# Optimization experiments

Measured on AMD Instinct MI355X. Metric: run time of the kernel, lower is better.

Reference implementation:

```python
import jax, jax.numpy as jnp
import numpy as np

N = 50000      # nodes
E = 500000     # edges
IN = 128       # input feature dim
HID = 64       # hidden per-head dim
CLS = 64       # num classes
SLOPE = 0.2    # leaky_relu negative slope


def _gat_layer(x, W, al, ar, src, dst):
    """One GATConv: project, per-edge score, edge-softmax over dst, weighted aggregate.
    x: [N, Din], W: [Din, H*F], al/ar: [H, F]. Returns [N, H, F]."""
    H, F = al.shape
    n = x.shape[0]
    feat = (x @ W).reshape(n, H, F)                      # [N,H,F]
    el = jnp.einsum('nhf,hf->nh', feat, al)              # [N,H]
    er = jnp.einsum('nhf,hf->nh', feat, ar)              # [N,H]
    e = el[src] + er[dst]                                # u_add_v -> [E,H]
    e = jnp.where(e >= 0, e, SLOPE * e)                  # leaky_relu
    # edge_softmax over destination nodes (numerically stable)
    m = jax.lax.stop_gradient(jax.ops.segment_max(e, dst, num_segments=n))
    ex = jnp.exp(e - m[dst])
    denom = jax.ops.segment_sum(ex, dst, num_segments=n)
    a = ex / denom[dst]                                  # [E,H]
    # u_mul_e + sum aggregation
    out = jax.ops.segment_sum(feat[src] * a[:, :, None], dst, num_segments=n)
    return out                                           # [N,H,F]


def setup_inputs() -> dict:
    key = jax.random.key(0)
    ks = jax.random.split(key, 12)
    s = 0.05  # xavier-ish scale
    x = jax.random.normal(ks[0], (N, IN), jnp.float32)
    src = jax.random.randint(ks[1], (E,), 0, N)
    dst = jax.random.randint(ks[2], (E,), 0, N)
    W1 = jax.random.normal(ks[3], (IN, 4 * HID), jnp.float32) * s
    al1 = jax.random.normal(ks[4], (4, HID), jnp.float32) * s
    ar1 = jax.random.normal(ks[5], (4, HID), jnp.float32) * s
    W2 = jax.random.normal(ks[6], (4 * HID, 4 * HID), jnp.float32) * s
    al2 = jax.random.normal(ks[7], (4, HID), jnp.float32) * s
    ar2 = jax.random.normal(ks[8], (4, HID), jnp.float32) * s
    W3 = jax.random.normal(ks[9], (4 * HID, CLS), jnp.float32) * s
    al3 = jax.random.normal(ks[10], (1, CLS), jnp.float32) * s
    ar3 = jax.random.normal(ks[11], (1, CLS), jnp.float32) * s
    res_W3 = jax.random.normal(jax.random.fold_in(key, 99), (4 * HID, CLS), jnp.float32) * s
    return {"x": x, "W1": W1, "al1": al1, "ar1": ar1, "W2": W2, "al2": al2,
            "ar2": ar2, "W3": W3, "al3": al3, "ar3": ar3, "res_W3": res_W3,
            "src": src, "dst": dst}


def reference(x, W1, al1, ar1, W2, al2, ar2, W3, al3, ar3, res_W3, src, dst):
    # layer 0: no residual, elu activation, flatten heads
    h = _gat_layer(x, W1, al1, ar1, src, dst)            # [N,4,64]
    h = jax.nn.elu(h).reshape(N, -1)                     # [N,256]
    # layer 1: residual is Identity (in_dst 256 == 4*64), elu, flatten
    h1 = _gat_layer(h, W2, al2, ar2, src, dst)           # [N,4,64]
    h1 = h1 + h.reshape(N, 4, HID)                       # residual (Identity)
    h = jax.nn.elu(h1).reshape(N, -1)                    # [N,256]
    # layer 2: residual Linear 256->64, no activation, mean over heads
    h2 = _gat_layer(h, W3, al3, ar3, src, dst)           # [N,1,64]
    h2 = h2 + (h @ res_W3).reshape(N, 1, CLS)            # residual fc
    logits = h2.mean(axis=1)                             # [N,64]
    return logits
```

## Files before the change

### kernel.cpp

```cpp
#include <hip/hip_runtime.h>
#include <hip/hip_bf16.h>
#include <math.h>

#define SLOPE 0.2f

typedef __attribute__((ext_vector_type(8))) short short8;
typedef __attribute__((ext_vector_type(4))) float f32x4;

static __device__ __forceinline__ float leakyf(float x) { return x >= 0.f ? x : SLOPE * x; }
static __device__ __forceinline__ float bflo(unsigned u) { return __builtin_bit_cast(float, u << 16); }
static __device__ __forceinline__ float bfhi(unsigned u) { return __builtin_bit_cast(float, u & 0xffff0000u); }
static __device__ __forceinline__ unsigned short f2bf(float f) {
    unsigned u = __builtin_bit_cast(unsigned, f);
    return (unsigned short)((u + 0x7fff + ((u >> 16) & 1)) >> 16);
}

struct __align__(8) us4 { unsigned short a, b, c, d; };

__global__ __launch_bounds__(256) void tconv_all(const float* __restrict__ W1,
                                                 const float* __restrict__ W2,
                                                 const float* __restrict__ W3,
                                                 const float* __restrict__ rW3,
                                                 unsigned short* __restrict__ W1t,
                                                 unsigned short* __restrict__ W2t,
                                                 unsigned short* __restrict__ W3c) {
    int i = blockIdx.x * 256 + threadIdx.x;
    const float* W; unsigned short* Wt; int K, lNc, idx;
    if (i < 32768)       { W = W1;  Wt = W1t;            K = 128; lNc = 8; idx = i; }
    else if (i < 98304)  { W = W2;  Wt = W2t;            K = 256; lNc = 8; idx = i - 32768; }
    else if (i < 114688) { W = W3;  Wt = W3c;            K = 256; lNc = 6; idx = i - 98304; }
    else                 { W = rW3; Wt = W3c + 64 * 256; K = 256; lNc = 6; idx = i - 114688; }
    int k = idx >> lNc, n = idx & ((1 << lNc) - 1);
    Wt[n * K + k] = f2bf(W[idx]);
}

template<bool A_F32>
__global__ __launch_bounds__(256) void gemm_l12(const void* __restrict__ Av,
                                                const unsigned short* __restrict__ Wt,
                                                unsigned short* __restrict__ outb,
                                                const float* __restrict__ al,
                                                const float* __restrict__ ar,
                                                float* __restrict__ el,
                                                float* __restrict__ er,
                                                int M, int K) {
    const int lane = threadIdx.x & 63;
    const int wid = threadIdx.x >> 6;
    const int rlo = lane & 15;
    const int q = lane >> 4;
    const int kg = q * 8;
    const int m0 = blockIdx.x * 64;
    const int cbase = wid * 64;

    f32x4 acc[4][4];
#pragma unroll
    for (int mf = 0; mf < 4; ++mf)
#pragma unroll
        for (int nf = 0; nf < 4; ++nf) acc[mf][nf] = (f32x4){0.f, 0.f, 0.f, 0.f};

    for (int k0 = 0; k0 < K; k0 += 32) {
        short8 a[4];
#pragma unroll
        for (int mf = 0; mf < 4; ++mf) {
            int r = m0 + mf * 16 + rlo;
            if (r >= M) r = M - 1;
            if (A_F32) {
                const float* ap = (const float*)Av + (size_t)r * K + k0 + kg;
                float4 f0 = *(const float4*)ap;
                float4 f1 = *(const float4*)(ap + 4);
                short8 t;
                t[0] = f2bf(f0.x); t[1] = f2bf(f0.y); t[2] = f2bf(f0.z); t[3] = f2bf(f0.w);
                t[4] = f2bf(f1.x); t[5] = f2bf(f1.y); t[6] = f2bf(f1.z); t[7] = f2bf(f1.w);
                a[mf] = t;
            } else {
                a[mf] = *(const short8*)((const unsigned short*)Av + (size_t)r * K + k0 + kg);
            }
        }
#pragma unroll
        for (int nf = 0; nf < 4; ++nf) {
            short8 b = *(const short8*)(Wt + (size_t)(cbase + nf * 16 + rlo) * K + k0 + kg);
#pragma unroll
            for (int mf = 0; mf < 4; ++mf)
                acc[mf][nf] = __builtin_amdgcn_mfma_f32_16x16x32_bf16(a[mf], b, acc[mf][nf], 0, 0, 0);
        }
    }

    float alv[4], arv[4];
#pragma unroll
    for (int nf = 0; nf < 4; ++nf) {
        alv[nf] = al[cbase + nf * 16 + rlo];
        arv[nf] = ar[cbase + nf * 16 + rlo];
    }

#pragma unroll
    for (int mf = 0; mf < 4; ++mf) {
#pragma unroll
        for (int reg = 0; reg < 4; ++reg) {
            int r = m0 + mf * 16 + q * 4 + reg;
            float pl = 0.f, pr = 0.f;
#pragma unroll
            for (int nf = 0; nf < 4; ++nf) {
                pl += acc[mf][nf][reg] * alv[nf];
                pr += acc[mf][nf][reg] * arv[nf];
            }
#pragma unroll
            for (int off = 1; off < 16; off <<= 1) {
                pl += __shfl_xor(pl, off);
                pr += __shfl_xor(pr, off);
            }
            if (rlo == 0 && r < M) {
                el[(size_t)r * 4 + wid] = pl;
                er[(size_t)r * 4 + wid] = pr;
            }
            if (r < M) {
#pragma unroll
                for (int nf = 0; nf < 4; ++nf)
                    outb[(size_t)r * 256 + cbase + nf * 16 + rlo] = f2bf(acc[mf][nf][reg]);
            }
        }
    }
}

__global__ __launch_bounds__(256) void gemm_l3(const unsigned short* __restrict__ A,
                                               const unsigned short* __restrict__ Wt,
                                               unsigned short* __restrict__ featb,
                                               float* __restrict__ resf,
                                               const float* __restrict__ al,
                                               const float* __restrict__ ar,
                                               float* __restrict__ el,
                                               float* __restrict__ er, int M) {
    const int K = 256;
    const int lane = threadIdx.x & 63;
    const int wid = threadIdx.x >> 6;
    const int rlo = lane & 15;
    const int q = lane >> 4;
    const int kg = q * 8;
    const int m0 = blockIdx.x * 128 + (wid >> 1) * 64;
    const int ch = wid & 1;
    const int cbase = ch * 64;

    f32x4 acc[4][4];
#pragma unroll
    for (int mf = 0; mf < 4; ++mf)
#pragma unroll
        for (int nf = 0; nf < 4; ++nf) acc[mf][nf] = (f32x4){0.f, 0.f, 0.f, 0.f};

    for (int k0 = 0; k0 < K; k0 += 32) {
        short8 a[4];
#pragma unroll
        for (int mf = 0; mf < 4; ++mf) {
            int r = m0 + mf * 16 + rlo;
            if (r >= M) r = M - 1;
            a[mf] = *(const short8*)(A + (size_t)r * K + k0 + kg);
        }
#pragma unroll
        for (int nf = 0; nf < 4; ++nf) {
            short8 b = *(const short8*)(Wt + (size_t)(cbase + nf * 16 + rlo) * K + k0 + kg);
#pragma unroll
            for (int mf = 0; mf < 4; ++mf)
                acc[mf][nf] = __builtin_amdgcn_mfma_f32_16x16x32_bf16(a[mf], b, acc[mf][nf], 0, 0, 0);
        }
    }

    float alv[4], arv[4];
    if (ch == 0) {
#pragma unroll
        for (int nf = 0; nf < 4; ++nf) {
            alv[nf] = al[nf * 16 + rlo];
            arv[nf] = ar[nf * 16 + rlo];
        }
    }

#pragma unroll
    for (int mf = 0; mf < 4; ++mf) {
#pragma unroll
        for (int reg = 0; reg < 4; ++reg) {
            int r = m0 + mf * 16 + q * 4 + reg;
            if (ch == 0) {
                float pl = 0.f, pr = 0.f;
#pragma unroll
                for (int nf = 0; nf < 4; ++nf) {
                    pl += acc[mf][nf][reg] * alv[nf];
                    pr += acc[mf][nf][reg] * arv[nf];
                }
#pragma unroll
                for (int off = 1; off < 16; off <<= 1) {
                    pl += __shfl_xor(pl, off);
                    pr += __shfl_xor(pr, off);
                }
                if (rlo == 0 && r < M) { el[r] = pl; er[r] = pr; }
                if (r < M) {
#pragma unroll
                    for (int nf = 0; nf < 4; ++nf)
                        featb[(size_t)r * 64 + nf * 16 + rlo] = f2bf(acc[mf][nf][reg]);
                }
            } else if (r < M) {
#pragma unroll
                for (int nf = 0; nf < 4; ++nf)
                    resf[(size_t)r * 64 + nf * 16 + rlo] = acc[mf][nf][reg];
            }
        }
    }
}

__global__ void hist_kernel(const int* __restrict__ dst, int* __restrict__ counts, int e) {
    int i = blockIdx.x * blockDim.x + threadIdx.x;
    if (i < e) atomicAdd(&counts[dst[i]], 1);
}

__global__ __launch_bounds__(1024) void scan_block(const int* __restrict__ counts,
                                                   int* __restrict__ offsets,
                                                   int* __restrict__ bsums, int n) {
    __shared__ int ws[16];
    int tid = threadIdx.x, lane = tid & 63, wid = tid >> 6;
    int idx = blockIdx.x * 1024 + tid;
    int v = (idx < n) ? counts[idx] : 0;
    int s = v;
#pragma unroll
    for (int off = 1; off < 64; off <<= 1) {
        int t = __shfl_up(s, off);
        if (lane >= off) s += t;
    }
    if (lane == 63) ws[wid] = s;
    __syncthreads();
    if (tid < 16) {
        int w2 = ws[tid];
#pragma unroll
        for (int off = 1; off < 16; off <<= 1) {
            int t = __shfl_up(w2, off);
            if (tid >= off) w2 += t;
        }
        ws[tid] = w2;
    }
    __syncthreads();
    int wpre = wid ? ws[wid - 1] : 0;
    if (idx < n) offsets[idx] = wpre + s - v;
    if (tid == 0) bsums[blockIdx.x] = ws[15];
}

__global__ __launch_bounds__(1024) void add_off(const int* __restrict__ bsums,
                                                int* __restrict__ offsets,
                                                int* __restrict__ cursor, int n, int e, int nb) {
    __shared__ int base_s;
    int tid = threadIdx.x;
    if (tid < 64) {
        int v = (tid < blockIdx.x && tid < nb) ? bsums[tid] : 0;
#pragma unroll
        for (int off = 32; off > 0; off >>= 1) v += __shfl_xor(v, off);
        if (tid == 0) base_s = v;
    }
    __syncthreads();
    int idx = blockIdx.x * 1024 + tid;
    if (idx < n) {
        int v = offsets[idx] + base_s;
        offsets[idx] = v;
        cursor[idx] = v;
    }
    if (idx == 0) offsets[n] = e;
}

__global__ void scatter_kernel(const int* __restrict__ src, const int* __restrict__ dst,
                               int* __restrict__ cursor, int* __restrict__ csr_src,
                               int* __restrict__ csr_dst, int e) {
    int i = blockIdx.x * blockDim.x + threadIdx.x;
    if (i < e) {
        int d = dst[i];
        int pos = atomicAdd(&cursor[d], 1);
        csr_src[pos] = src[i];
        csr_dst[pos] = d;
    }
}

template<int H>
__global__ __launch_bounds__(256) void edge_scores(const int* __restrict__ csr_src,
                                                   const int* __restrict__ csr_dst,
                                                   const float* __restrict__ el,
                                                   const float* __restrict__ er,
                                                   float* __restrict__ w, int E) {
    int e = blockIdx.x * 256 + threadIdx.x;
    if (e >= E) return;
    int s = csr_src[e], d = csr_dst[e];
    if (H == 4) {
        float4 l = *(const float4*)(el + (size_t)s * 4);
        float4 r = *(const float4*)(er + (size_t)d * 4);
        float4 o;
        o.x = __expf(fminf(leakyf(l.x + r.x), 80.f));
        o.y = __expf(fminf(leakyf(l.y + r.y), 80.f));
        o.z = __expf(fminf(leakyf(l.z + r.z), 80.f));
        o.w = __expf(fminf(leakyf(l.w + r.w), 80.f));
        *(float4*)(w + (size_t)e * 4) = o;
    } else {
        w[e] = __expf(fminf(leakyf(el[s] + er[d]), 80.f));
    }
}

template<int H, int RES, int ACT, bool OUT_BF16>
__global__ __launch_bounds__(256) void gat_agg(const unsigned short* __restrict__ fp,
                                               const float* __restrict__ wbuf,
                                               const int* __restrict__ offsets,
                                               const int* __restrict__ csr_src,
                                               const void* __restrict__ resid,
                                               void* __restrict__ outv, int n) {
    const int D = H * 64;
    int node = blockIdx.x * 4 + (threadIdx.x >> 6);
    int lane = threadIdx.x & 63;
    if (node >= n) return;
    int e0 = offsets[node], e1 = offsets[node + 1];
    const int hf = (H == 4) ? (lane >> 4) : 0;

    float den = 0.f;
    float acc[4] = {0.f, 0.f, 0.f, 0.f};

    for (int e = e0; e < e1; e += 8) {
        int s[8];
        float w[8];
#pragma unroll
        for (int j = 0; j < 8; ++j) {
            int idx = e + j;
            bool ok = idx < e1;
            int ii = ok ? idx : (e1 - 1);
            s[j] = csr_src[ii];
            float wv = (H == 4) ? wbuf[(size_t)ii * 4 + hf] : wbuf[ii];
            w[j] = ok ? wv : 0.f;
        }
        if (H == 4) {
            uint2 u[8];
#pragma unroll
            for (int j = 0; j < 8; ++j)
                u[j] = *(const uint2*)(fp + (size_t)s[j] * 256 + lane * 4);
#pragma unroll
            for (int j = 0; j < 8; ++j) {
                den += w[j];
                acc[0] += w[j] * bflo(u[j].x);
                acc[1] += w[j] * bfhi(u[j].x);
                acc[2] += w[j] * bflo(u[j].y);
                acc[3] += w[j] * bfhi(u[j].y);
            }
        } else {
            unsigned u[8];
#pragma unroll
            for (int j = 0; j < 8; ++j)
                u[j] = ((const unsigned short*)fp)[(size_t)s[j] * 64 + lane];
#pragma unroll
            for (int j = 0; j < 8; ++j) {
                den += w[j];
                acc[0] += w[j] * bflo(u[j]);
            }
        }
    }

    float inv = den > 0.f ? 1.f / den : 0.f;
    float v[4];
#pragma unroll
    for (int i = 0; i < 4; ++i) v[i] = acc[i] * inv;

    if (RES == 1) {
        uint2 ru = *(const uint2*)((const unsigned short*)resid + (size_t)node * D + lane * 4);
        v[0] += bflo(ru.x); v[1] += bfhi(ru.x); v[2] += bflo(ru.y); v[3] += bfhi(ru.y);
    } else if (RES == 2) {
        v[0] += ((const float*)resid)[(size_t)node * D + lane];
    }
    if (ACT == 1) {
#pragma unroll
        for (int i = 0; i < 4; ++i) v[i] = v[i] > 0.f ? v[i] : __expf(v[i]) - 1.f;
    }
    if (OUT_BF16) {
        if (H == 4) {
            us4 o = {f2bf(v[0]), f2bf(v[1]), f2bf(v[2]), f2bf(v[3])};
            *(us4*)((unsigned short*)outv + (size_t)node * D + lane * 4) = o;
        } else {
            ((unsigned short*)outv)[(size_t)node * D + lane] = f2bf(v[0]);
        }
    } else {
        if (H == 4) {
            float4 o = {v[0], v[1], v[2], v[3]};
            *(float4*)((float*)outv + (size_t)node * D + lane * 4) = o;
        } else {
            ((float*)outv)[(size_t)node * D + lane] = v[0];
        }
    }
}

extern "C" void kernel_launch(void* const* d_in, const int* in_sizes, int n_in,
                              void* d_out, int out_size, void* d_ws, size_t ws_size,
                              hipStream_t stream) {
    const float* x      = (const float*)d_in[0];
    const float* W1     = (const float*)d_in[1];
    const float* al1    = (const float*)d_in[2];
    const float* ar1    = (const float*)d_in[3];
    const float* W2     = (const float*)d_in[4];
    const float* al2    = (const float*)d_in[5];
    const float* ar2    = (const float*)d_in[6];
    const float* W3     = (const float*)d_in[7];
    const float* al3    = (const float*)d_in[8];
    const float* ar3    = (const float*)d_in[9];
    const float* res_W3 = (const float*)d_in[10];
    const int*   src    = (const int*)d_in[11];
    const int*   dst    = (const int*)d_in[12];

    const int N = in_sizes[0] / 128;
    const int E = in_sizes[11];

    float* out = (float*)d_out;

    unsigned short* featb = (unsigned short*)d_ws;
    unsigned short* h1    = featb + (size_t)N * 256;
    unsigned short* h2    = h1 + (size_t)N * 256;
    unsigned short* W1t   = h2 + (size_t)N * 256;
    unsigned short* W2t   = W1t + 256 * 128;
    unsigned short* W3c   = W2t + 256 * 256;
    float* resf = (float*)(W3c + 128 * 256);
    float* el   = resf + (size_t)N * 64;
    float* er   = el + (size_t)N * 4;
    float* wbuf = er + (size_t)N * 4;
    int* offsets = (int*)(wbuf + (size_t)E * 4);
    int* cursor  = offsets + (N + 1);
    int* csr_src = cursor + N;
    int* csr_dst = csr_src + E;
    int* bsums   = csr_dst + E;

    const int T = 256;
    const int scan_blocks = (N + 1023) / 1024;
    const int edge_blocks = (E + T - 1) / T;

    tconv_all<<<512, T, 0, stream>>>(W1, W2, W3, res_W3, W1t, W2t, W3c);

    hipMemsetAsync(cursor, 0, (size_t)N * sizeof(int), stream);
    hist_kernel<<<edge_blocks, T, 0, stream>>>(dst, cursor, E);
    scan_block<<<scan_blocks, 1024, 0, stream>>>(cursor, offsets, bsums, N);
    add_off<<<scan_blocks, 1024, 0, stream>>>(bsums, offsets, cursor, N, E, scan_blocks);
    scatter_kernel<<<edge_blocks, T, 0, stream>>>(src, dst, cursor, csr_src, csr_dst, E);

    int gemm12_blocks = (N + 63) / 64;
    int gemm3_blocks = (N + 127) / 128;
    int node_blocks = (N + 3) / 4;

    gemm_l12<true><<<gemm12_blocks, T, 0, stream>>>(x, W1t, featb, al1, ar1, el, er, N, 128);
    edge_scores<4><<<edge_blocks, T, 0, stream>>>(csr_src, csr_dst, el, er, wbuf, E);
    gat_agg<4, 0, 1, true><<<node_blocks, T, 0, stream>>>(featb, wbuf, offsets, csr_src, nullptr, h1, N);

    gemm_l12<false><<<gemm12_blocks, T, 0, stream>>>(h1, W2t, featb, al2, ar2, el, er, N, 256);
    edge_scores<4><<<edge_blocks, T, 0, stream>>>(csr_src, csr_dst, el, er, wbuf, E);
    gat_agg<4, 1, 1, true><<<node_blocks, T, 0, stream>>>(featb, wbuf, offsets, csr_src, h1, h2, N);

    gemm_l3<<<gemm3_blocks, T, 0, stream>>>(h2, W3c, featb, resf, al3, ar3, el, er, N);
    edge_scores<1><<<edge_blocks, T, 0, stream>>>(csr_src, csr_dst, el, er, wbuf, E);
    gat_agg<1, 2, 0, false><<<node_blocks, T, 0, stream>>>(featb, wbuf, offsets, csr_src, resf, out, N);
}
```

Baseline: 297.6 us.

## Permute feature column layout for vector stores and vectorize edge-score and aggregation loads

Permutes the K ordering of W2/W3/resW3 so GEMM epilogues can write four bf16 (or fp32) values per lane as one vector store, with the final output index unpermuted in the aggregation kernel. Edge scores now handle four edges per thread and store the weights head-major (planar [H][E]), so the aggregation kernel reads contiguous weights and source indices with 16-byte loads. Padding reads past segment ends depend on the buffer gap (offsets padded to N+8) and on E being a multiple of 4. The permuted column layout adds coupling between kernels and unaligned vector loads at arbitrary edge offsets.

Measured after the change: 287.9 us. 3.2% less time.

```diff
diff --git a/kernel.cpp b/kernel.cpp
--- a/kernel.cpp
+++ b/kernel.cpp
@@ -6,6 +6,7 @@
 
 typedef __attribute__((ext_vector_type(8))) short short8;
 typedef __attribute__((ext_vector_type(4))) float f32x4;
+typedef __attribute__((ext_vector_type(4))) int   i32x4;
 
 static __device__ __forceinline__ float leakyf(float x) { return x >= 0.f ? x : SLOPE * x; }
 static __device__ __forceinline__ float bflo(unsigned u) { return __builtin_bit_cast(float, u << 16); }
@@ -16,6 +17,7 @@
 }
 
 struct __align__(8) us4 { unsigned short a, b, c, d; };
+
 
 __global__ __launch_bounds__(256) void tconv_all(const float* __restrict__ W1,
                                                  const float* __restrict__ W2,
@@ -25,13 +27,14 @@
                                                  unsigned short* __restrict__ W2t,
                                                  unsigned short* __restrict__ W3c) {
     int i = blockIdx.x * 256 + threadIdx.x;
-    const float* W; unsigned short* Wt; int K, lNc, idx;
-    if (i < 32768)       { W = W1;  Wt = W1t;            K = 128; lNc = 8; idx = i; }
-    else if (i < 98304)  { W = W2;  Wt = W2t;            K = 256; lNc = 8; idx = i - 32768; }
-    else if (i < 114688) { W = W3;  Wt = W3c;            K = 256; lNc = 6; idx = i - 98304; }
-    else                 { W = rW3; Wt = W3c + 64 * 256; K = 256; lNc = 6; idx = i - 114688; }
+    const float* W; unsigned short* Wt; int K, lNc, idx; bool permK;
+    if (i < 32768)       { W = W1;  Wt = W1t;            K = 128; lNc = 8; idx = i;          permK = false; }
+    else if (i < 98304)  { W = W2;  Wt = W2t;            K = 256; lNc = 8; idx = i - 32768;  permK = true; }
+    else if (i < 114688) { W = W3;  Wt = W3c;            K = 256; lNc = 6; idx = i - 98304;  permK = true; }
+    else                 { W = rW3; Wt = W3c + 64 * 256; K = 256; lNc = 6; idx = i - 114688; permK = true; }
     int k = idx >> lNc, n = idx & ((1 << lNc) - 1);
-    Wt[n * K + k] = f2bf(W[idx]);
+    int kp = permK ? ((k & ~63) | (((k & 15) << 2) | ((k & 63) >> 4))) : k;
+    Wt[n * K + kp] = f2bf(W[idx]);
 }
 
 template<bool A_F32>
@@ -112,9 +115,9 @@
                 er[(size_t)r * 4 + wid] = pr;
             }
             if (r < M) {
-#pragma unroll
-                for (int nf = 0; nf < 4; ++nf)
-                    outb[(size_t)r * 256 + cbase + nf * 16 + rlo] = f2bf(acc[mf][nf][reg]);
+                us4 o = {f2bf(acc[mf][0][reg]), f2bf(acc[mf][1][reg]),
+                         f2bf(acc[mf][2][reg]), f2bf(acc[mf][3][reg])};
+                *(us4*)(outb + (size_t)r * 256 + cbase + rlo * 4) = o;
             }
         }
     }
@@ -189,14 +192,13 @@
                 }
                 if (rlo == 0 && r < M) { el[r] = pl; er[r] = pr; }
                 if (r < M) {
-#pragma unroll
-                    for (int nf = 0; nf < 4; ++nf)
-                        featb[(size_t)r * 64 + nf * 16 + rlo] = f2bf(acc[mf][nf][reg]);
+                    us4 o = {f2bf(acc[mf][0][reg]), f2bf(acc[mf][1][reg]),
+                             f2bf(acc[mf][2][reg]), f2bf(acc[mf][3][reg])};
+                    *(us4*)(featb + (size_t)r * 64 + rlo * 4) = o;
                 }
             } else if (r < M) {
-#pragma unroll
-                for (int nf = 0; nf < 4; ++nf)
-                    resf[(size_t)r * 64 + nf * 16 + rlo] = acc[mf][nf][reg];
+                float4 o = {acc[mf][0][reg], acc[mf][1][reg], acc[mf][2][reg], acc[mf][3][reg]};
+                *(float4*)(resf + (size_t)r * 64 + rlo * 4) = o;
             }
         }
     }
@@ -276,20 +278,32 @@
                                                    const float* __restrict__ el,
                                                    const float* __restrict__ er,
                                                    float* __restrict__ w, int E) {
-    int e = blockIdx.x * 256 + threadIdx.x;
-    if (e >= E) return;
-    int s = csr_src[e], d = csr_dst[e];
+    int e4 = (blockIdx.x * 256 + threadIdx.x) * 4;
+    if (e4 >= E) return;
+    i32x4 s = *(const i32x4*)(csr_src + e4);
+    i32x4 d = *(const i32x4*)(csr_dst + e4);
     if (H == 4) {
-        float4 l = *(const float4*)(el + (size_t)s * 4);
-        float4 r = *(const float4*)(er + (size_t)d * 4);
+        float4 o0, o1, o2, o3;
+        float* op[4] = {&o0.x, &o1.x, &o2.x, &o3.x};
+#pragma unroll
+        for (int j = 0; j < 4; ++j) {
+            float4 l = *(const float4*)(el + (size_t)s[j] * 4);
+            float4 r = *(const float4*)(er + (size_t)d[j] * 4);
+            op[0][j] = __expf(fminf(leakyf(l.x + r.x), 80.f));
+            op[1][j] = __expf(fminf(leakyf(l.y + r.y), 80.f));
+            op[2][j] = __expf(fminf(leakyf(l.z + r.z), 80.f));
+            op[3][j] = __expf(fminf(leakyf(l.w + r.w), 80.f));
+        }
+        *(float4*)(w + 0 * (size_t)E + e4) = o0;
+        *(float4*)(w + 1 * (size_t)E + e4) = o1;
+        *(float4*)(w + 2 * (size_t)E + e4) = o2;
+        *(float4*)(w + 3 * (size_t)E + e4) = o3;
+    } else {
         float4 o;
-        o.x = __expf(fminf(leakyf(l.x + r.x), 80.f));
-        o.y = __expf(fminf(leakyf(l.y + r.y), 80.f));
-        o.z = __expf(fminf(leakyf(l.z + r.z), 80.f));
-        o.w = __expf(fminf(leakyf(l.w + r.w), 80.f));
-        *(float4*)(w + (size_t)e * 4) = o;
-    } else {
-        w[e] = __expf(fminf(leakyf(el[s] + er[d]), 80.f));
+#pragma unroll
+        for (int j = 0; j < 4; ++j)
+            (&o.x)[j] = __expf(fminf(leakyf(el[s[j]] + er[d[j]]), 80.f));
+        *(float4*)(w + e4) = o;
     }
 }
 
@@ -299,28 +313,34 @@
                                                const int* __restrict__ offsets,
                                                const int* __restrict__ csr_src,
                                                const void* __restrict__ resid,
-                                               void* __restrict__ outv, int n) {
+                                               void* __restrict__ outv, int n, int E) {
     const int D = H * 64;
     int node = blockIdx.x * 4 + (threadIdx.x >> 6);
     int lane = threadIdx.x & 63;
     if (node >= n) return;
     int e0 = offsets[node], e1 = offsets[node + 1];
     const int hf = (H == 4) ? (lane >> 4) : 0;
+    const float* wb = wbuf + (size_t)hf * E;
 
     float den = 0.f;
     float acc[4] = {0.f, 0.f, 0.f, 0.f};
 
     for (int e = e0; e < e1; e += 8) {
+        i32x4 sv0, sv1;
+        f32x4 wv0, wv1;
+        __builtin_memcpy(&sv0, csr_src + e, 16);
+        __builtin_memcpy(&sv1, csr_src + e + 4, 16);
+        __builtin_memcpy(&wv0, wb + e, 16);
+        __builtin_memcpy(&wv1, wb + e + 4, 16);
         int s[8];
         float w[8];
 #pragma unroll
         for (int j = 0; j < 8; ++j) {
-            int idx = e + j;
-            bool ok = idx < e1;
-            int ii = ok ? idx : (e1 - 1);
-            s[j] = csr_src[ii];
-            float wv = (H == 4) ? wbuf[(size_t)ii * 4 + hf] : wbuf[ii];
-            w[j] = ok ? wv : 0.f;
+            bool ok = (e + j) < e1;
+            int sj = (j < 4) ? sv0[j] : sv1[j - 4];
+            float wj = (j < 4) ? wv0[j] : wv1[j - 4];
+            s[j] = ok ? sj : 0;
+            w[j] = ok ? wj : 0.f;
         }
         if (H == 4) {
             uint2 u[8];
@@ -339,7 +359,7 @@
             unsigned u[8];
 #pragma unroll
             for (int j = 0; j < 8; ++j)
-                u[j] = ((const unsigned short*)fp)[(size_t)s[j] * 64 + lane];
+                u[j] = fp[(size_t)s[j] * 64 + lane];
 #pragma unroll
             for (int j = 0; j < 8; ++j) {
                 den += w[j];
@@ -375,7 +395,8 @@
             float4 o = {v[0], v[1], v[2], v[3]};
             *(float4*)((float*)outv + (size_t)node * D + lane * 4) = o;
         } else {
-            ((float*)outv)[(size_t)node * D + lane] = v[0];
+            int c = (lane & 3) * 16 + (lane >> 2);
+            ((float*)outv)[(size_t)node * D + c] = v[0];
         }
     }
 }
@@ -413,7 +434,7 @@
     float* er   = el + (size_t)N * 4;
     float* wbuf = er + (size_t)N * 4;
     int* offsets = (int*)(wbuf + (size_t)E * 4);
-    int* cursor  = offsets + (N + 1);
+    int* cursor  = offsets + (N + 8);
     int* csr_src = cursor + N;
     int* csr_dst = csr_src + E;
     int* bsums   = csr_dst + E;
@@ -421,6 +442,7 @@
     const int T = 256;
     const int scan_blocks = (N + 1023) / 1024;
     const int edge_blocks = (E + T - 1) / T;
+    const int es_blocks = (E / 4 + T - 1) / T;
 
     tconv_all<<<512, T, 0, stream>>>(W1, W2, W3, res_W3, W1t, W2t, W3c);
 
@@ -435,14 +457,14 @@
     int node_blocks = (N + 3) / 4;
 
     gemm_l12<true><<<gemm12_blocks, T, 0, stream>>>(x, W1t, featb, al1, ar1, el, er, N, 128);
-    edge_scores<4><<<edge_blocks, T, 0, stream>>>(csr_src, csr_dst, el, er, wbuf, E);
-    gat_agg<4, 0, 1, true><<<node_blocks, T, 0, stream>>>(featb, wbuf, offsets, csr_src, nullptr, h1, N);
+    edge_scores<4><<<es_blocks, T, 0, stream>>>(csr_src, csr_dst, el, er, wbuf, E);
+    gat_agg<4, 0, 1, true><<<node_blocks, T, 0, stream>>>(featb, wbuf, offsets, csr_src, nullptr, h1, N, E);
 
     gemm_l12<false><<<gemm12_blocks, T, 0, stream>>>(h1, W2t, featb, al2, ar2, el, er, N, 256);
-    edge_scores<4><<<edge_blocks, T, 0, stream>>>(csr_src, csr_dst, el, er, wbuf, E);
-    gat_agg<4, 1, 1, true><<<node_blocks, T, 0, stream>>>(featb, wbuf, offsets, csr_src, h1, h2, N);
+    edge_scores<4><<<es_blocks, T, 0, stream>>>(csr_src, csr_dst, el, er, wbuf, E);
+    gat_agg<4, 1, 1, true><<<node_blocks, T, 0, stream>>>(featb, wbuf, offsets, csr_src, h1, h2, N, E);
 
     gemm_l3<<<gemm3_blocks, T, 0, stream>>>(h2, W3c, featb, resf, al3, ar3, el, er, N);
-    edge_scores<1><<<edge_blocks, T, 0, stream>>>(csr_src, csr_dst, el, er, wbuf, E);
-    gat_agg<1, 2, 0, false><<<node_blocks, T, 0, stream>>>(featb, wbuf, offsets, csr_src, resf, out, N);
-}
+    edge_scores<1><<<es_blocks, T, 0, stream>>>(csr_src, csr_dst, el, er, wbuf, E);
+    gat_agg<1, 2, 0, false><<<node_blocks, T, 0, stream>>>(featb, wbuf, offsets, csr_src, resf, out, N, E);
+}
```
